# Performance work log

Hardware: AMD Instinct MI355X
Metric: run time of the kernel (lower is better)

The kernel has to match this reference:

```python
import jax, jax.numpy as jnp
import numpy as np

B, S, H, CHAR_DIM, VOCAB = 32, 2048, 1024, 256, 64


def setup_inputs() -> dict:
    key = jax.random.key(0)
    ks = jax.random.split(key, 16)
    scale = 0.02
    char = jax.random.randint(ks[0], (B,), 0, VOCAB)
    h_prev = jax.random.normal(ks[1], (1, B, H), jnp.float32)
    c_prev = jax.random.normal(ks[2], (1, B, H), jnp.float32)
    encoder_lens = jnp.maximum(jax.random.randint(ks[3], (B,), 0, S), 1)
    encoder_hidden_states = jax.random.normal(ks[4], (B, S, H), jnp.float32)
    embedding = jax.random.normal(ks[5], (VOCAB, CHAR_DIM), jnp.float32) * scale
    w_ih = jax.random.normal(ks[6], (4 * H, CHAR_DIM), jnp.float32) * scale
    w_hh = jax.random.normal(ks[7], (4 * H, H), jnp.float32) * scale
    b_ih = jax.random.normal(ks[8], (4 * H,), jnp.float32) * scale
    b_hh = jax.random.normal(ks[9], (4 * H,), jnp.float32) * scale
    attn_w = jax.random.normal(ks[10], (2 * H,), jnp.float32) * scale
    attn_b = jax.random.normal(ks[11], (1,), jnp.float32) * scale
    concat_w = jax.random.normal(ks[12], (H, 2 * H), jnp.float32) * scale
    concat_b = jax.random.normal(ks[13], (H,), jnp.float32) * scale
    out_w = jax.random.normal(ks[14], (VOCAB, H), jnp.float32) * scale
    out_b = jax.random.normal(ks[15], (VOCAB,), jnp.float32) * scale
    return dict(char=char, h_prev=h_prev, c_prev=c_prev, encoder_lens=encoder_lens,
                encoder_hidden_states=encoder_hidden_states, embedding=embedding,
                w_ih=w_ih, w_hh=w_hh, b_ih=b_ih, b_hh=b_hh,
                attn_w=attn_w, attn_b=attn_b, concat_w=concat_w, concat_b=concat_b,
                out_w=out_w, out_b=out_b)


def reference(char, h_prev, c_prev, encoder_lens, encoder_hidden_states,
              embedding, w_ih, w_hh, b_ih, b_hh, attn_w, attn_b,
              concat_w, concat_b, out_w, out_b):
    Hd = h_prev.shape[-1]
    seq = encoder_hidden_states.shape[1]

    # --- embedding lookup (padding_idx rows are just zero-init in training; lookup is identical) ---
    x = embedding[char]  # (B, char_dim)

    # --- single-step, single-layer LSTM cell (PyTorch gate order: i, f, g, o) ---
    z = x @ w_ih.T + b_ih + h_prev[0] @ w_hh.T + b_hh  # (B, 4H)
    i, f, g, o = jnp.split(z, 4, axis=-1)
    c_new = jax.nn.sigmoid(f) * c_prev[0] + jax.nn.sigmoid(i) * jnp.tanh(g)
    h_new = jax.nn.sigmoid(o) * jnp.tanh(c_new)  # (B, H)

    # --- additive attention: Linear(concat([enc, hid]), 1) == enc@w_enc + hid@w_hid + b ---
    w_enc, w_hid = attn_w[:Hd], attn_w[Hd:]
    logits = jnp.einsum('bsh,h->bs', encoder_hidden_states, w_enc) \
             + (h_new @ w_hid)[:, None] + attn_b[0]  # (B, S)
    mask = jnp.arange(seq)[None, :] < encoder_lens[:, None]
    logits = jnp.where(mask, logits, jnp.float32(-1e9))
    attn = jax.nn.softmax(logits, axis=-1)  # (B, S)

    # --- context and output ---
    context = jnp.einsum('bs,bsh->bh', attn, encoder_hidden_states)  # (B, H)
    nh = jnp.tanh(jnp.concatenate([context, h_new], axis=-1) @ concat_w.T + concat_b)
    output_logits = nh @ out_w.T + out_b  # (B, vocab)
    return output_logits, h_new[None], c_new[None]
```

## Files before the change

### kernel.cpp

```cpp
#include <hip/hip_runtime.h>
#include <math.h>

#define NB    32
#define SEQ   2048
#define HD    1024
#define CDIM  256
#define NATTN 512
#define RECU  516

__device__ __forceinline__ float dot4(float4 a, float4 b) {
    return a.x*b.x + a.y*b.y + a.z*b.z + a.w*b.w;
}
__device__ __forceinline__ unsigned short f2bf(float f) {
    unsigned int u = __float_as_uint(f);
    u += 0x7FFFu + ((u >> 16) & 1u);
    return (unsigned short)(u >> 16);
}
__device__ __forceinline__ float bf2f(unsigned short s) {
    return __uint_as_float(((unsigned int)s) << 16);
}

__device__ void attn_wave(int wid, const float* __restrict__ enc,
                          const int* __restrict__ lens, const float* __restrict__ attn_w,
                          unsigned int* __restrict__ partU)
{
    int b = wid & 31, j = wid >> 5;
    int lane = threadIdx.x & 63;
    int len  = lens[b];

    float4 we0 = *(const float4*)(attn_w       + lane * 4);
    float4 we1 = *(const float4*)(attn_w + 256 + lane * 4);
    float4 we2 = *(const float4*)(attn_w + 512 + lane * 4);
    float4 we3 = *(const float4*)(attn_w + 768 + lane * 4);
    float4 c0 = make_float4(0,0,0,0), c1 = c0, c2 = c0, c3 = c0;
    float l = 0.f;

    const float* ebase = enc + (size_t)b * SEQ * HD + lane * 4;
    for (int s = j; s < len; s += 64) {
        const float* ep = ebase + (size_t)s * HD;
        float4 e0 = *(const float4*)(ep);
        float4 e1 = *(const float4*)(ep + 256);
        float4 e2 = *(const float4*)(ep + 512);
        float4 e3 = *(const float4*)(ep + 768);
        float v = dot4(e0,we0) + dot4(e1,we1) + dot4(e2,we2) + dot4(e3,we3);
        #pragma unroll
        for (int off = 32; off > 0; off >>= 1) v += __shfl_xor(v, off, 64);
        float p = __expf(v);
        l += p;
        c0.x += p*e0.x; c0.y += p*e0.y; c0.z += p*e0.z; c0.w += p*e0.w;
        c1.x += p*e1.x; c1.y += p*e1.y; c1.z += p*e1.z; c1.w += p*e1.w;
        c2.x += p*e2.x; c2.y += p*e2.y; c2.z += p*e2.z; c2.w += p*e2.w;
        c3.x += p*e3.x; c3.y += p*e3.y; c3.z += p*e3.z; c3.w += p*e3.w;
    }
    unsigned short* rec = (unsigned short*)(partU + (size_t)(b * 64 + j) * RECU);
    *(ushort4*)(rec +       lane * 4) = make_ushort4(f2bf(c0.x), f2bf(c0.y), f2bf(c0.z), f2bf(c0.w));
    *(ushort4*)(rec + 256 + lane * 4) = make_ushort4(f2bf(c1.x), f2bf(c1.y), f2bf(c1.z), f2bf(c1.w));
    *(ushort4*)(rec + 512 + lane * 4) = make_ushort4(f2bf(c2.x), f2bf(c2.y), f2bf(c2.z), f2bf(c2.w));
    *(ushort4*)(rec + 768 + lane * 4) = make_ushort4(f2bf(c3.x), f2bf(c3.y), f2bf(c3.z), f2bf(c3.w));
    if (lane == 0) *(float*)(rec + 1024) = l;
}

__device__ void gemm0_body(int gid,
                           const float* __restrict__ emb, const int* __restrict__ chars,
                           const float* __restrict__ h_prev,
                           const float* __restrict__ w_ih, const float* __restrict__ w_hh,
                           float* __restrict__ zpart)
{
    __shared__ float Xs[32][36];
    __shared__ float Ws[32][132];

    const int nt = gid & 31;
    const int ky = gid >> 5;
    const int n0 = nt * 128;
    const int kbase = ky * 160;

    const int t  = threadIdx.x;
    const int nn = t & 31;
    const int bb = t >> 5;

    float4 acc0 = make_float4(0,0,0,0), acc1 = acc0, acc2 = acc0, acc3 = acc0;

    const int xb = t >> 3, xk = (t & 7) * 4;
    const int wn = t >> 3, wk = (t & 7) * 4;

    for (int k0 = kbase; k0 < kbase + 160; k0 += 32) {
        {
            int k = k0 + xk;
            float4 xv;
            if (k < CDIM) xv = *(const float4*)(emb + chars[xb] * CDIM + k);
            else          xv = *(const float4*)(h_prev + xb * HD + (k - CDIM));
            Xs[xk+0][xb] = xv.x; Xs[xk+1][xb] = xv.y; Xs[xk+2][xb] = xv.z; Xs[xk+3][xb] = xv.w;
        }
        #pragma unroll
        for (int i = 0; i < 4; ++i) {
            int n = n0 + wn + 32 * i;
            int k = k0 + wk;
            float4 wv;
            if (k < CDIM) wv = *(const float4*)(w_ih + n * CDIM + k);
            else          wv = *(const float4*)(w_hh + n * HD + (k - CDIM));
            int nc = wn + 32 * i;
            Ws[wk+0][nc] = wv.x; Ws[wk+1][nc] = wv.y; Ws[wk+2][nc] = wv.z; Ws[wk+3][nc] = wv.w;
        }
        __syncthreads();
        #pragma unroll
        for (int k = 0; k < 32; ++k) {
            float4 xv = *(const float4*)&Xs[k][bb * 4];
            float4 wv = *(const float4*)&Ws[k][nn * 4];
            acc0.x += xv.x*wv.x; acc0.y += xv.x*wv.y; acc0.z += xv.x*wv.z; acc0.w += xv.x*wv.w;
            acc1.x += xv.y*wv.x; acc1.y += xv.y*wv.y; acc1.z += xv.y*wv.z; acc1.w += xv.y*wv.w;
            acc2.x += xv.z*wv.x; acc2.y += xv.z*wv.y; acc2.z += xv.z*wv.z; acc2.w += xv.z*wv.w;
            acc3.x += xv.w*wv.x; acc3.y += xv.w*wv.y; acc3.z += xv.w*wv.z; acc3.w += xv.w*wv.w;
        }
        __syncthreads();
    }
    float* zr = zpart + (size_t)(ky * 32 + bb * 4) * 4096 + n0 + nn * 4;
    *(float4*)(zr           ) = acc0;
    *(float4*)(zr + 4096    ) = acc1;
    *(float4*)(zr + 4096 * 2) = acc2;
    *(float4*)(zr + 4096 * 3) = acc3;
}

__global__ void __launch_bounds__(256) attn_gemm0(
    const float* __restrict__ enc, const int* __restrict__ lens,
    const float* __restrict__ attn_w, unsigned int* __restrict__ partU,
    const float* __restrict__ emb, const int* __restrict__ chars,
    const float* __restrict__ h_prev,
    const float* __restrict__ w_ih, const float* __restrict__ w_hh,
    float* __restrict__ zpart)
{
    if (blockIdx.x < NATTN)
        attn_wave(blockIdx.x * 4 + (threadIdx.x >> 6), enc, lens, attn_w, partU);
    else
        gemm0_body(blockIdx.x - NATTN, emb, chars, h_prev, w_ih, w_hh, zpart);
}

__global__ void gates_combine(const float* __restrict__ zpart,
                              const float* __restrict__ b_ih, const float* __restrict__ b_hh,
                              const float* __restrict__ c_prev,
                              const unsigned int* __restrict__ partU,
                              float* __restrict__ d_out, float* __restrict__ xcat2)
{
    int t = threadIdx.x;
    if (blockIdx.x < 128) {
        int idx = blockIdx.x * 256 + t;
        int b = idx >> 10, j = idx & 1023;
        float z[4];
        #pragma unroll
        for (int g = 0; g < 4; ++g) {
            int n = g * 1024 + j;
            float v = b_ih[n] + b_hh[n];
            #pragma unroll
            for (int s = 0; s < 8; ++s) v += zpart[(size_t)(s * 32 + b) * 4096 + n];
            z[g] = v;
        }
        float gi = 1.f / (1.f + __expf(-z[0]));
        float gf = 1.f / (1.f + __expf(-z[1]));
        float gg = tanhf(z[2]);
        float go = 1.f / (1.f + __expf(-z[3]));
        float c = gf * c_prev[idx] + gi * gg;
        float h = go * tanhf(c);
        d_out[2048 + idx]         = h;
        d_out[2048 + 32768 + idx] = c;
        xcat2[b * 2048 + 1024 + j] = h;
    } else {
        int bid = blockIdx.x - 128;
        int b = bid >> 2, slice = bid & 3;
        int hh = slice * 256 + t;
        const unsigned int* pbase = partU + (size_t)b * 64 * RECU;
        float a0 = 0.f, a1 = 0.f, a2 = 0.f, a3 = 0.f;
        float l0 = 0.f, l1 = 0.f, l2 = 0.f, l3 = 0.f;
        #pragma unroll
        for (int i = 0; i < 64; i += 4) {
            const unsigned short* r0 = (const unsigned short*)(pbase + (size_t)(i+0) * RECU);
            const unsigned short* r1 = (const unsigned short*)(pbase + (size_t)(i+1) * RECU);
            const unsigned short* r2 = (const unsigned short*)(pbase + (size_t)(i+2) * RECU);
            const unsigned short* r3 = (const unsigned short*)(pbase + (size_t)(i+3) * RECU);
            a0 += bf2f(r0[hh]);  l0 += *(const float*)(r0 + 1024);
            a1 += bf2f(r1[hh]);  l1 += *(const float*)(r1 + 1024);
            a2 += bf2f(r2[hh]);  l2 += *(const float*)(r2 + 1024);
            a3 += bf2f(r3[hh]);  l3 += *(const float*)(r3 + 1024);
        }
        xcat2[b * 2048 + hh] = (a0 + a1 + a2 + a3) / (l0 + l1 + l2 + l3);
    }
}

__global__ void __launch_bounds__(256) gemm_concat(
    const float* __restrict__ xcat2, const float* __restrict__ concat_w,
    float* __restrict__ nhpart)
{
    __shared__ float Xs[32][36];
    __shared__ float Ws[32][68];

    const int gid = blockIdx.x;
    const int nt = gid & 15;
    const int ky = gid >> 4;
    const int n0 = nt * 64;
    const int kbase = ky * 128;

    const int t  = threadIdx.x;
    const int nn = t & 15;
    const int bb = t >> 4;

    float4 acc0 = make_float4(0,0,0,0), acc1 = acc0;

    const int xb = t >> 3, xk = (t & 7) * 4;
    const int wn = t >> 2, wk = (t & 3) * 8;

    float4 xv_p  = *(const float4*)(xcat2 + xb * 2048 + kbase + xk);
    float4 wv_p0 = *(const float4*)(concat_w + (n0 + wn) * 2048 + kbase + wk);
    float4 wv_p1 = *(const float4*)(concat_w + (n0 + wn) * 2048 + kbase + wk + 4);

    #pragma unroll
    for (int it = 0; it < 4; ++it) {
        Xs[xk+0][xb] = xv_p.x; Xs[xk+1][xb] = xv_p.y; Xs[xk+2][xb] = xv_p.z; Xs[xk+3][xb] = xv_p.w;
        Ws[wk+0][wn] = wv_p0.x; Ws[wk+1][wn] = wv_p0.y; Ws[wk+2][wn] = wv_p0.z; Ws[wk+3][wn] = wv_p0.w;
        Ws[wk+4][wn] = wv_p1.x; Ws[wk+5][wn] = wv_p1.y; Ws[wk+6][wn] = wv_p1.z; Ws[wk+7][wn] = wv_p1.w;
        __syncthreads();
        if (it < 3) {
            int k0n = kbase + (it + 1) * 32;
            xv_p  = *(const float4*)(xcat2 + xb * 2048 + k0n + xk);
            wv_p0 = *(const float4*)(concat_w + (n0 + wn) * 2048 + k0n + wk);
            wv_p1 = *(const float4*)(concat_w + (n0 + wn) * 2048 + k0n + wk + 4);
        }
        #pragma unroll
        for (int k = 0; k < 32; ++k) {
            float2 xv = *(const float2*)&Xs[k][bb * 2];
            float4 wv = *(const float4*)&Ws[k][nn * 4];
            acc0.x += xv.x*wv.x; acc0.y += xv.x*wv.y; acc0.z += xv.x*wv.z; acc0.w += xv.x*wv.w;
            acc1.x += xv.y*wv.x; acc1.y += xv.y*wv.y; acc1.z += xv.y*wv.z; acc1.w += xv.y*wv.w;
        }
        __syncthreads();
    }
    float* nr = nhpart + (size_t)(ky * 32 + bb * 2) * 1024 + n0 + nn * 4;
    *(float4*)(nr       ) = acc0;
    *(float4*)(nr + 1024) = acc1;
}

__global__ void __launch_bounds__(256) k_nh_out(
    const float* __restrict__ nhpart, const float* __restrict__ concat_b,
    const float* __restrict__ out_w, const float* __restrict__ out_b,
    float* __restrict__ d_out)
{
    __shared__ float nhl[1024];
    int u = blockIdx.x;
    int b = u >> 3, vg = u & 7;
    int t = threadIdx.x;
    #pragma unroll
    for (int j = 0; j < 4; ++j) {
        int n = t + j * 256;
        float v = concat_b[n];
        #pragma unroll
        for (int s = 0; s < 16; ++s) v += nhpart[(size_t)(s * 32 + b) * 1024 + n];
        nhl[n] = tanhf(v);
    }
    __syncthreads();
    int w = t >> 6, lane = t & 63;
    const float* nr = nhl + lane * 4;
    #pragma unroll
    for (int vv = 0; vv < 2; ++vv) {
        int v = vg * 8 + w * 2 + vv;
        const float* wr = out_w + v * 1024 + lane * 4;
        float acc = 0.f;
        #pragma unroll
        for (int i = 0; i < 4; ++i) {
            float4 wv = *(const float4*)(wr + i * 256);
            float4 nv = *(const float4*)(nr + i * 256);
            acc += dot4(wv, nv);
        }
        #pragma unroll
        for (int off = 32; off > 0; off >>= 1) acc += __shfl_xor(acc, off, 64);
        if (lane == 0) d_out[b * 64 + v] = acc + out_b[v];
    }
}

extern "C" void kernel_launch(void* const* d_in, const int* in_sizes, int n_in,
                              void* d_out, int out_size, void* d_ws, size_t ws_size,
                              hipStream_t stream)
{
    const int*   chars    = (const int*)  d_in[0];
    const float* h_prev   = (const float*)d_in[1];
    const float* c_prev   = (const float*)d_in[2];
    const int*   lens     = (const int*)  d_in[3];
    const float* enc      = (const float*)d_in[4];
    const float* emb      = (const float*)d_in[5];
    const float* w_ih     = (const float*)d_in[6];
    const float* w_hh     = (const float*)d_in[7];
    const float* b_ih     = (const float*)d_in[8];
    const float* b_hh     = (const float*)d_in[9];
    const float* attn_w   = (const float*)d_in[10];
    const float* concat_w = (const float*)d_in[12];
    const float* concat_b = (const float*)d_in[13];
    const float* out_w    = (const float*)d_in[14];
    const float* out_b    = (const float*)d_in[15];
    float* out = (float*)d_out;

    float* ws = (float*)d_ws;
    float*        zpart  = ws;
    float*        xcat2  = zpart + 1048576;
    unsigned int* partU  = (unsigned int*)(xcat2 + 65536);
    float*        nhpart = (float*)(partU + 1056768);

    attn_gemm0<<<dim3(NATTN + 256), 256, 0, stream>>>(enc, lens, attn_w, partU,
                                                      emb, chars, h_prev, w_ih, w_hh, zpart);
    gates_combine<<<dim3(256), 256, 0, stream>>>(zpart, b_ih, b_hh, c_prev, partU, out, xcat2);
    gemm_concat<<<dim3(256), 256, 0, stream>>>(xcat2, concat_w, nhpart);
    k_nh_out<<<dim3(256), 256, 0, stream>>>(nhpart, concat_b, out_w, out_b, out);
}
```

Baseline: 49.62 us.

## Fuse tail kernels into one persistent kernel with grid-wide barriers

Merges the gates/context-combine, concat GEMM and output-projection kernels into a single 256-block kernel. The stages are separated by atomic-counter grid barriers instead of separate kernel launches. This removes two launch gaps and their drain/refill overhead. In exchange it adds a memset launch and spin-wait barriers, and it relies on all 256 blocks being co-resident to avoid deadlock.

```diff
diff --git a/kernel.cpp b/kernel.cpp
--- a/kernel.cpp
+++ b/kernel.cpp
@@ -18,6 +18,19 @@
 }
 __device__ __forceinline__ float bf2f(unsigned short s) {
     return __uint_as_float(((unsigned int)s) << 16);
+}
+
+__device__ __forceinline__ void grid_barrier(int* ctr, int target)
+{
+    __threadfence();
+    __syncthreads();
+    if (threadIdx.x == 0) {
+        __hip_atomic_fetch_add(ctr, 1, __ATOMIC_ACQ_REL, __HIP_MEMORY_SCOPE_AGENT);
+        while (__hip_atomic_load(ctr, __ATOMIC_ACQUIRE, __HIP_MEMORY_SCOPE_AGENT) < target)
+            __builtin_amdgcn_s_sleep(2);
+    }
+    __syncthreads();
+    __threadfence();
 }
 
 __device__ void attn_wave(int wid, const float* __restrict__ enc,
@@ -134,15 +147,21 @@
         gemm0_body(blockIdx.x - NATTN, emb, chars, h_prev, w_ih, w_hh, zpart);
 }
 
-__global__ void gates_combine(const float* __restrict__ zpart,
-                              const float* __restrict__ b_ih, const float* __restrict__ b_hh,
-                              const float* __restrict__ c_prev,
-                              const unsigned int* __restrict__ partU,
-                              float* __restrict__ d_out, float* __restrict__ xcat2)
-{
-    int t = threadIdx.x;
-    if (blockIdx.x < 128) {
-        int idx = blockIdx.x * 256 + t;
+__global__ void __launch_bounds__(256) tail_fused(
+    const float* __restrict__ zpart,
+    const float* __restrict__ b_ih, const float* __restrict__ b_hh,
+    const float* __restrict__ c_prev, const unsigned int* __restrict__ partU,
+    float* __restrict__ xcat2,
+    const float* __restrict__ concat_w, float* __restrict__ nhpart,
+    const float* __restrict__ concat_b,
+    const float* __restrict__ out_w, const float* __restrict__ out_b,
+    float* __restrict__ d_out, int* __restrict__ bar)
+{
+    __shared__ float smem[32*36 + 32*68];
+    const int bid = blockIdx.x, t = threadIdx.x;
+
+    if (bid < 128) {
+        int idx = bid * 256 + t;
         int b = idx >> 10, j = idx & 1023;
         float z[4];
         #pragma unroll
@@ -163,8 +182,8 @@
         d_out[2048 + 32768 + idx] = c;
         xcat2[b * 2048 + 1024 + j] = h;
     } else {
-        int bid = blockIdx.x - 128;
-        int b = bid >> 2, slice = bid & 3;
+        int u = bid - 128;
+        int b = u >> 2, slice = u & 3;
         int hh = slice * 256 + t;
         const unsigned int* pbase = partU + (size_t)b * 64 * RECU;
         float a0 = 0.f, a1 = 0.f, a2 = 0.f, a3 = 0.f;
@@ -182,94 +201,87 @@
         }
         xcat2[b * 2048 + hh] = (a0 + a1 + a2 + a3) / (l0 + l1 + l2 + l3);
     }
-}
-
-__global__ void __launch_bounds__(256) gemm_concat(
-    const float* __restrict__ xcat2, const float* __restrict__ concat_w,
-    float* __restrict__ nhpart)
-{
-    __shared__ float Xs[32][36];
-    __shared__ float Ws[32][68];
-
-    const int gid = blockIdx.x;
-    const int nt = gid & 15;
-    const int ky = gid >> 4;
-    const int n0 = nt * 64;
-    const int kbase = ky * 128;
-
-    const int t  = threadIdx.x;
-    const int nn = t & 15;
-    const int bb = t >> 4;
-
-    float4 acc0 = make_float4(0,0,0,0), acc1 = acc0;
-
-    const int xb = t >> 3, xk = (t & 7) * 4;
-    const int wn = t >> 2, wk = (t & 3) * 8;
-
-    float4 xv_p  = *(const float4*)(xcat2 + xb * 2048 + kbase + xk);
-    float4 wv_p0 = *(const float4*)(concat_w + (n0 + wn) * 2048 + kbase + wk);
-    float4 wv_p1 = *(const float4*)(concat_w + (n0 + wn) * 2048 + kbase + wk + 4);
-
-    #pragma unroll
-    for (int it = 0; it < 4; ++it) {
-        Xs[xk+0][xb] = xv_p.x; Xs[xk+1][xb] = xv_p.y; Xs[xk+2][xb] = xv_p.z; Xs[xk+3][xb] = xv_p.w;
-        Ws[wk+0][wn] = wv_p0.x; Ws[wk+1][wn] = wv_p0.y; Ws[wk+2][wn] = wv_p0.z; Ws[wk+3][wn] = wv_p0.w;
-        Ws[wk+4][wn] = wv_p1.x; Ws[wk+5][wn] = wv_p1.y; Ws[wk+6][wn] = wv_p1.z; Ws[wk+7][wn] = wv_p1.w;
+
+    grid_barrier(bar + 0, 256);
+
+    {
+        float (*Xs)[36] = (float(*)[36])smem;
+        float (*Ws)[68] = (float(*)[68])(smem + 32*36);
+
+        const int nt = bid & 15;
+        const int ky = bid >> 4;
+        const int n0 = nt * 64;
+        const int kbase = ky * 128;
+
+        const int nn = t & 15;
+        const int bb = t >> 4;
+
+        float4 acc0 = make_float4(0,0,0,0), acc1 = acc0;
+
+        const int xb = t >> 3, xk = (t & 7) * 4;
+        const int wn = t >> 2, wk = (t & 3) * 8;
+
+        float4 xv_p  = *(const float4*)(xcat2 + xb * 2048 + kbase + xk);
+        float4 wv_p0 = *(const float4*)(concat_w + (n0 + wn) * 2048 + kbase + wk);
+        float4 wv_p1 = *(const float4*)(concat_w + (n0 + wn) * 2048 + kbase + wk + 4);
+
+        #pragma unroll
+        for (int it = 0; it < 4; ++it) {
+            Xs[xk+0][xb] = xv_p.x; Xs[xk+1][xb] = xv_p.y; Xs[xk+2][xb] = xv_p.z; Xs[xk+3][xb] = xv_p.w;
+            Ws[wk+0][wn] = wv_p0.x; Ws[wk+1][wn] = wv_p0.y; Ws[wk+2][wn] = wv_p0.z; Ws[wk+3][wn] = wv_p0.w;
+            Ws[wk+4][wn] = wv_p1.x; Ws[wk+5][wn] = wv_p1.y; Ws[wk+6][wn] = wv_p1.z; Ws[wk+7][wn] = wv_p1.w;
+            __syncthreads();
+            if (it < 3) {
+                int k0n = kbase + (it + 1) * 32;
+                xv_p  = *(const float4*)(xcat2 + xb * 2048 + k0n + xk);
+                wv_p0 = *(const float4*)(concat_w + (n0 + wn) * 2048 + k0n + wk);
+                wv_p1 = *(const float4*)(concat_w + (n0 + wn) * 2048 + k0n + wk + 4);
+            }
+            #pragma unroll
+            for (int k = 0; k < 32; ++k) {
+                float2 xv = *(const float2*)&Xs[k][bb * 2];
+                float4 wv = *(const float4*)&Ws[k][nn * 4];
+                acc0.x += xv.x*wv.x; acc0.y += xv.x*wv.y; acc0.z += xv.x*wv.z; acc0.w += xv.x*wv.w;
+                acc1.x += xv.y*wv.x; acc1.y += xv.y*wv.y; acc1.z += xv.y*wv.z; acc1.w += xv.y*wv.w;
+            }
+            __syncthreads();
+        }
+        float* nr = nhpart + (size_t)(ky * 32 + bb * 2) * 1024 + n0 + nn * 4;
+        *(float4*)(nr       ) = acc0;
+        *(float4*)(nr + 1024) = acc1;
+    }
+
+    grid_barrier(bar + 1, 256);
+
+    {
+        float* nhl = smem;
+        int b = bid >> 3, vg = bid & 7;
+        #pragma unroll
+        for (int j = 0; j < 4; ++j) {
+            int n = t + j * 256;
+            float v = concat_b[n];
+            #pragma unroll
+            for (int s = 0; s < 16; ++s) v += nhpart[(size_t)(s * 32 + b) * 1024 + n];
+            nhl[n] = tanhf(v);
+        }
         __syncthreads();
-        if (it < 3) {
-            int k0n = kbase + (it + 1) * 32;
-            xv_p  = *(const float4*)(xcat2 + xb * 2048 + k0n + xk);
-            wv_p0 = *(const float4*)(concat_w + (n0 + wn) * 2048 + k0n + wk);
-            wv_p1 = *(const float4*)(concat_w + (n0 + wn) * 2048 + k0n + wk + 4);
-        }
-        #pragma unroll
-        for (int k = 0; k < 32; ++k) {
-            float2 xv = *(const float2*)&Xs[k][bb * 2];
-            float4 wv = *(const float4*)&Ws[k][nn * 4];
-            acc0.x += xv.x*wv.x; acc0.y += xv.x*wv.y; acc0.z += xv.x*wv.z; acc0.w += xv.x*wv.w;
-            acc1.x += xv.y*wv.x; acc1.y += xv.y*wv.y; acc1.z += xv.y*wv.z; acc1.w += xv.y*wv.w;
-        }
-        __syncthreads();
-    }
-    float* nr = nhpart + (size_t)(ky * 32 + bb * 2) * 1024 + n0 + nn * 4;
-    *(float4*)(nr       ) = acc0;
-    *(float4*)(nr + 1024) = acc1;
-}
-
-__global__ void __launch_bounds__(256) k_nh_out(
-    const float* __restrict__ nhpart, const float* __restrict__ concat_b,
-    const float* __restrict__ out_w, const float* __restrict__ out_b,
-    float* __restrict__ d_out)
-{
-    __shared__ float nhl[1024];
-    int u = blockIdx.x;
-    int b = u >> 3, vg = u & 7;
-    int t = threadIdx.x;
-    #pragma unroll
-    for (int j = 0; j < 4; ++j) {
-        int n = t + j * 256;
-        float v = concat_b[n];
-        #pragma unroll
-        for (int s = 0; s < 16; ++s) v += nhpart[(size_t)(s * 32 + b) * 1024 + n];
-        nhl[n] = tanhf(v);
-    }
-    __syncthreads();
-    int w = t >> 6, lane = t & 63;
-    const float* nr = nhl + lane * 4;
-    #pragma unroll
-    for (int vv = 0; vv < 2; ++vv) {
-        int v = vg * 8 + w * 2 + vv;
-        const float* wr = out_w + v * 1024 + lane * 4;
-        float acc = 0.f;
-        #pragma unroll
-        for (int i = 0; i < 4; ++i) {
-            float4 wv = *(const float4*)(wr + i * 256);
-            float4 nv = *(const float4*)(nr + i * 256);
-            acc += dot4(wv, nv);
-        }
-        #pragma unroll
-        for (int off = 32; off > 0; off >>= 1) acc += __shfl_xor(acc, off, 64);
-        if (lane == 0) d_out[b * 64 + v] = acc + out_b[v];
+        int w = t >> 6, lane = t & 63;
+        const float* nr = nhl + lane * 4;
+        #pragma unroll
+        for (int vv = 0; vv < 2; ++vv) {
+            int v = vg * 8 + w * 2 + vv;
+            const float* wr = out_w + v * 1024 + lane * 4;
+            float acc = 0.f;
+            #pragma unroll
+            for (int i = 0; i < 4; ++i) {
+                float4 wv = *(const float4*)(wr + i * 256);
+                float4 nv = *(const float4*)(nr + i * 256);
+                acc += dot4(wv, nv);
+            }
+            #pragma unroll
+            for (int off = 32; off > 0; off >>= 1) acc += __shfl_xor(acc, off, 64);
+            if (lane == 0) d_out[b * 64 + v] = acc + out_b[v];
+        }
     }
 }
 
@@ -299,10 +311,13 @@
     float*        xcat2  = zpart + 1048576;
     unsigned int* partU  = (unsigned int*)(xcat2 + 65536);
     float*        nhpart = (float*)(partU + 1056768);
+    int*          bar    = (int*)(nhpart + 524288);
+
+    hipMemsetAsync(bar, 0, 2 * sizeof(int), stream);
 
     attn_gemm0<<<dim3(NATTN + 256), 256, 0, stream>>>(enc, lens, attn_w, partU,
                                                       emb, chars, h_prev, w_ih, w_hh, zpart);
-    gates_combine<<<dim3(256), 256, 0, stream>>>(zpart, b_ih, b_hh, c_prev, partU, out, xcat2);
-    gemm_concat<<<dim3(256), 256, 0, stream>>>(xcat2, concat_w, nhpart);
-    k_nh_out<<<dim3(256), 256, 0, stream>>>(nhpart, concat_b, out_w, out_b, out);
-}
+    tail_fused<<<dim3(256), 256, 0, stream>>>(zpart, b_ih, b_hh, c_prev, partU, xcat2,
+                                              concat_w, nhpart, concat_b, out_w, out_b,
+                                              out, bar);
+}
```

Result: slower. 157.1 us (+216.7%).
